# Kernel tuning notes

Measured on AMD Instinct MI355X. Metric: run time of the kernel, lower is better.

Reference implementation:

```python
import jax, jax.numpy as jnp
import numpy as np

B, NUM_ANCHORS, NUM_CLASSES = 32, 15130, 81
SCALE_XY, SCALE_WH = 0.1, 0.2
CRITERIA, MAX_OUT, SCORE_THRESH = 0.5, 200, 0.05


def setup_inputs() -> dict:
    key = jax.random.key(0)
    k1, k2, k3, k4 = jax.random.split(key, 4)
    ploc = jax.random.normal(k1, (B, 4, NUM_ANCHORS), dtype=jnp.float32)
    plabel = jax.random.normal(k2, (B, NUM_CLASSES, NUM_ANCHORS), dtype=jnp.float32)
    # default boxes in (cx, cy, w, h) form, all in [0, 1]
    xy = jax.random.uniform(k3, (NUM_ANCHORS, 2), dtype=jnp.float32, minval=0.05, maxval=0.95)
    wh = jax.random.uniform(k4, (NUM_ANCHORS, 2), dtype=jnp.float32, minval=0.02, maxval=0.3)
    dboxes_xywh = jnp.concatenate([xy, wh], axis=-1)
    return {"ploc": ploc, "plabel": plabel, "dboxes_xywh": dboxes_xywh}


def _iou(a, b):
    # a: [M,4] ltrb, b: [K,4] ltrb -> [M,K]
    lt = jnp.maximum(a[:, None, :2], b[None, :, :2])
    rb = jnp.minimum(a[:, None, 2:], b[None, :, 2:])
    wh = jnp.clip(rb - lt, 0.0)
    inter = wh[..., 0] * wh[..., 1]
    area_a = (a[:, 2] - a[:, 0]) * (a[:, 3] - a[:, 1])
    area_b = (b[:, 2] - b[:, 0]) * (b[:, 3] - b[:, 1])
    return inter / (area_a[:, None] + area_b[None, :] - inter + 1e-12)


def _decode(ploc, plabel, dboxes_xywh):
    # scale_back_batch: ploc [B,4,N] -> ltrb boxes [B,N,4]
    b = jnp.transpose(ploc, (0, 2, 1))
    xy = b[..., :2] * SCALE_XY * dboxes_xywh[:, 2:] + dboxes_xywh[:, :2]
    wh = jnp.exp(b[..., 2:] * SCALE_WH) * dboxes_xywh[:, 2:]
    ltrb = jnp.concatenate([xy - 0.5 * wh, xy + 0.5 * wh], axis=-1)  # [B,N,4]
    probs = jnp.transpose(jax.nn.softmax(plabel, axis=1), (0, 2, 1))  # [B,N,C]
    return ltrb, probs


def _nms_per_class(scores_c, boxes):
    # scores_c: [N], boxes: [N,4]
    s = jnp.where(scores_c > SCORE_THRESH, scores_c, 0.0)
    vals, idx = jax.lax.top_k(s, MAX_OUT)  # descending, matches score-sorted greedy order
    bx = boxes[idx]  # [MAX_OUT,4]
    iou = _iou(bx, bx)  # [MAX_OUT,MAX_OUT]
    later = jnp.arange(MAX_OUT)

    def body(i, keep):
        active = keep[i] & (vals[i] > 0.0)
        suppress = active & (iou[i] >= CRITERIA) & (later > i)
        return keep & ~suppress

    keep = jax.lax.fori_loop(0, MAX_OUT, body, jnp.ones((MAX_OUT,), bool))
    keep = keep & (vals > 0.0)
    return jnp.where(keep, vals, 0.0), bx


def _decode_single(probs_i, boxes_i):
    # skip background class 0
    cls_scores = probs_i[:, 1:].T  # [C-1, N]
    vals, bx = jax.vmap(_nms_per_class, in_axes=(0, None))(cls_scores, boxes_i)
    c1 = NUM_CLASSES - 1
    flat_v = vals.reshape(-1)                 # [(C-1)*MAX_OUT]
    flat_b = bx.reshape(-1, 4)
    labels = jnp.repeat(jnp.arange(1, c1 + 1, dtype=jnp.int32), MAX_OUT)
    top_v, top_i = jax.lax.top_k(flat_v, MAX_OUT)
    return flat_b[top_i], labels[top_i], top_v


def reference(ploc, plabel, dboxes_xywh):
    ltrb, probs = _decode(ploc, plabel, dboxes_xywh)
    boxes_out, labels_out, scores_out = jax.vmap(_decode_single)(probs, ltrb)
    return boxes_out, labels_out, scores_out
```

## Files before the change

### kernel.cpp

```cpp
#include <hip/hip_runtime.h>
#include <math.h>

namespace {
constexpr int BATCH = 32;
constexpr int NANCH = 15130;
constexpr int NCLS  = 81;
constexpr int C1    = 80;
constexpr int MAXO  = 200;
constexpr int APB   = 256;
constexpr int NBLKA = (NANCH + APB - 1) / APB;
constexpr int CAPK2 = 512;
constexpr int CAP   = 1024;
constexpr int CAPB  = 768;
constexpr int NBIN  = 2048;
constexpr int NBINK2 = 768;
constexpr unsigned BINBASE = 0x3D000000u;
constexpr int IMGCAP = C1 * MAXO;
}

#define SCORE_TH 0.05f
#define IOU_TH   0.5f

typedef unsigned long long u64;

__device__ __forceinline__ u64 shflx64(u64 v, int mask) {
    int lo = __shfl_xor((int)(unsigned)(v & 0xffffffffull), mask, 64);
    int hi = __shfl_xor((int)(unsigned)(v >> 32), mask, 64);
    return ((u64)(unsigned)hi << 32) | (unsigned)lo;
}

__device__ __forceinline__ void bitonic_desc(u64* keys, int P,
                                             int tid, int nthr) {
    for (int k = 2; k <= P; k <<= 1) {
        for (int j = k >> 1; j > 0; j >>= 1) {
            for (int i = tid; i < P; i += nthr) {
                int ixj = i ^ j;
                if (ixj > i) {
                    u64 a = keys[i], c = keys[ixj];
                    bool up = ((i & k) == 0);
                    if (up ? (a < c) : (a > c)) { keys[i] = c; keys[ixj] = a; }
                }
            }
            __syncthreads();
        }
    }
}

__device__ __forceinline__ u64 regsort256(u64 key, u64* lds, int tid) {
    for (int k = 2; k <= 256; k <<= 1) {
        for (int j = k >> 1; j > 0; j >>= 1) {
            u64 pv;
            if (j < 64) {
                pv = shflx64(key, j);
            } else {
                lds[tid] = key;
                __syncthreads();
                pv = lds[tid ^ j];
            }
            bool up = ((tid & k) == 0);
            bool lt = ((tid & j) == 0);
            u64 mx = (key > pv) ? key : pv;
            u64 mn = (key > pv) ? pv : key;
            key = (up == lt) ? mx : mn;
            if (j >= 64) __syncthreads();
        }
    }
    return key;
}

__device__ __forceinline__ void iou_parts(const float4 bb, const float aa,
                                          const float4 bi, const float ai,
                                          float& in_, float& dn) {
#pragma clang fp contract(off)
    float l = fmaxf(bi.x, bb.x);
    float t = fmaxf(bi.y, bb.y);
    float r = fminf(bi.z, bb.z);
    float d = fminf(bi.w, bb.w);
    in_ = fmaxf(r - l, 0.f) * fmaxf(d - t, 0.f);
    dn  = ai + aa - in_ + 1e-12f;
}

__global__ __launch_bounds__(256, 3) void ssd_decode_stats(
    const float* __restrict__ ploc, const float* __restrict__ plabel,
    const float* __restrict__ dboxes,
    float* __restrict__ ltrb, float* __restrict__ rowmax,
    float* __restrict__ rowsum,
    int* __restrict__ cntg, u64* __restrict__ bucket) {
#pragma clang fp contract(off)
    __shared__ int lcnt[C1], lbase[C1], lrank[C1];

    const int tid = threadIdx.x;
    const int b   = blockIdx.x / NBLKA;
    const int n0  = (blockIdx.x % NBLKA) * APB;
    const int n   = n0 + tid;
    const bool act = (n < NANCH);

    if (tid < C1) lcnt[tid] = 0;

    float x[NCLS];
    float s = 1.f;
    u64 w0 = 0, w1 = 0;
    if (act) {
        const float* pl = ploc + (size_t)b * 4 * NANCH + n;
        float px = pl[0], py = pl[NANCH], pw = pl[2 * NANCH],
              ph = pl[3 * NANCH];
        float4 db = reinterpret_cast<const float4*>(dboxes)[n];
        float cx = px * 0.1f * db.z + db.x;
        float cy = py * 0.1f * db.w + db.y;
        float w  = expf(pw * 0.2f) * db.z;
        float h  = expf(ph * 0.2f) * db.w;
        float4 o;
        o.x = cx - 0.5f * w; o.y = cy - 0.5f * h;
        o.z = cx + 0.5f * w; o.w = cy + 0.5f * h;
        reinterpret_cast<float4*>(ltrb)[(size_t)b * NANCH + n] = o;

        const float* pb = plabel + (size_t)b * NCLS * NANCH + n;
#pragma unroll
        for (int c = 0; c < NCLS; ++c) x[c] = pb[(size_t)c * NANCH];

        float m = -INFINITY;
#pragma unroll
        for (int c = 0; c < NCLS; ++c) m = fmaxf(m, x[c]);
#pragma unroll
        for (int c = 0; c < NCLS; ++c) x[c] = expf(x[c] - m);
        s = 0.f;
#pragma unroll
        for (int c = 0; c < NCLS; ++c) s += x[c];
        rowmax[(size_t)b * NANCH + n] = m;
        rowsum[(size_t)b * NANCH + n] = s;

        const float sc = s * SCORE_TH;
        const float lo = sc * 0.99999952f;
        const float hi = sc * 1.00000048f;
#pragma unroll
        for (int c = 1; c < NCLS; ++c) {
            float e = x[c];
            bool band = (e >= lo) && (e <= hi);
            bool pass = (e > hi);
            if (__any(band)) pass = band ? ((e / s) > SCORE_TH) : pass;
            if (pass) {
                atomicAdd(&lcnt[c - 1], 1);
                if (c <= 64) w0 |= 1ull << (c - 1);
                else         w1 |= 1ull << (c - 65);
            }
        }
    }
    __syncthreads();

    if (tid < C1) {
        int cn = lcnt[tid];
        lbase[tid] = (cn > 0) ? atomicAdd(&cntg[b * C1 + tid], cn) : 0;
        lrank[tid] = 0;
    }
    __syncthreads();

    if (act) {
#pragma unroll
        for (int c = 1; c < NCLS; ++c) {
            bool pass = (c <= 64) ? ((w0 >> (c - 1)) & 1ull)
                                  : ((w1 >> (c - 65)) & 1ull);
            if (pass) {
                int r = atomicAdd(&lrank[c - 1], 1);
                int pos = lbase[c - 1] + r;
                if (pos < CAPB) {
                    float p = x[c] / s;
                    bucket[(size_t)(b * C1 + (c - 1)) * CAPB + pos] =
                        ((u64)__float_as_uint(p) << 32)
                        | (u64)(0xFFFFFFFFu - (unsigned)n);
                }
            }
        }
    }
}

__global__ __launch_bounds__(64) void ssd_class_nms(
    const float* __restrict__ plabel, const float* __restrict__ rowmax,
    const float* __restrict__ rowsum, const float* __restrict__ ltrb,
    const int* __restrict__ cntg, const u64* __restrict__ bucket,
    float* __restrict__ pcVals, float* __restrict__ pcBoxes,
    int* __restrict__ imgcnt, u64* __restrict__ imglist) {
    __shared__ u64 pool[MAXO * 4];
    __shared__ __align__(16) u64 candbox[CAPK2];
    __shared__ int cnt, cutbin;

    unsigned* hist = (unsigned*)pool;
    u64* cand = candbox;
    float4* box4 = reinterpret_cast<float4*>(candbox);
    float* areas = reinterpret_cast<float*>(candbox) + 800;

    const int lane = threadIdx.x;
    const int b    = blockIdx.x / C1;
    const int cls  = blockIdx.x % C1 + 1;
    const int bc   = b * C1 + (cls - 1);

    for (int i = lane; i < NBINK2; i += 64) hist[i] = 0u;
    if (lane == 0) { cnt = 0; cutbin = 1; }
    __syncthreads();

    const float* pl = plabel + ((size_t)b * NCLS + cls) * NANCH;
    const float* rm = rowmax + (size_t)b * NANCH;
    const float* rs = rowsum + (size_t)b * NANCH;
    const u64* bkt = bucket + (size_t)bc * CAPB;

    const int gcount = cntg[bc];
    const bool ovf = (gcount > CAPB);
    int gathered;

    if (!ovf) {
        for (int i = lane; i < gcount; i += 64) {
            unsigned bits = (unsigned)(bkt[i] >> 32);
            unsigned bin = ((bits - BINBASE) >> 16) + 1u;
            if (bin > NBINK2 - 1) bin = NBINK2 - 1;
            atomicAdd(&hist[bin], 1u);
        }
        __syncthreads();

        const int base = lane * 12;
        int loc = 0;
#pragma unroll
        for (int k = 0; k < 12; ++k) loc += (int)hist[base + k];
        int sfx = loc;
        for (int off = 1; off < 64; off <<= 1) {
            int t = __shfl_down(sfx, off, 64);
            if (lane + off < 64) sfx += t;
        }
        const int nztot = __shfl(sfx, 0);
        {
            int S = sfx - loc;
            for (int k = 11; k >= 0; --k) {
                int binv = (int)hist[base + k];
                int Sk = S + binv;
                int bin = base + k;
                if (bin >= 1 && Sk >= MAXO && S < MAXO) cutbin = bin;
                S = Sk;
            }
        }
        __syncthreads();
        const int B = (nztot >= MAXO) ? cutbin : 1;

        for (int i = lane; i < gcount; i += 64) {
            u64 k = bkt[i];
            unsigned bits = (unsigned)(k >> 32);
            unsigned bin = ((bits - BINBASE) >> 16) + 1u;
            if (bin > NBINK2 - 1) bin = NBINK2 - 1;
            if ((int)bin >= B) {
                int pos = atomicAdd(&cnt, 1);
                if (pos < CAPK2) cand[pos] = k;
            }
        }
        __syncthreads();
        gathered = min(cnt, CAPK2);
    } else {
        for (int n = lane; n < NANCH; n += 64) {
            float p = expf(pl[n] - rm[n]) / rs[n];
            if (p > SCORE_TH) {
                int pos = atomicAdd(&cnt, 1);
                if (pos < CAPK2)
                    cand[pos] = ((u64)__float_as_uint(p) << 32)
                              | (u64)(0xFFFFFFFFu - (unsigned)n);
            }
        }
        __syncthreads();
        gathered = min(cnt, CAPK2);
    }

    u64 r0, r1, r2, r3;
    if (gathered <= 256) {
        r0 = (lane < gathered) ? cand[lane] : 0ull;
        r1 = (64 + lane < gathered) ? cand[64 + lane] : 0ull;
        r2 = (128 + lane < gathered) ? cand[128 + lane] : 0ull;
        r3 = (192 + lane < gathered) ? cand[192 + lane] : 0ull;

        auto SH = [&](u64& rr, int j, bool up) {
            u64 pv = shflx64(rr, j);
            bool lt = ((lane & j) == 0);
            u64 mx = (rr > pv) ? rr : pv;
            u64 mn = (rr > pv) ? pv : rr;
            rr = (up == lt) ? mx : mn;
        };
        auto CE = [](u64& a, u64& c, bool up) {
            u64 mx = (a > c) ? a : c;
            u64 mn = (a > c) ? c : a;
            a = up ? mx : mn;
            c = up ? mn : mx;
        };
        for (int k = 2; k <= 32; k <<= 1) {
            for (int j = k >> 1; j > 0; j >>= 1) {
                bool up = ((lane & k) == 0);
                SH(r0, j, up); SH(r1, j, up); SH(r2, j, up); SH(r3, j, up);
            }
        }
        for (int j = 32; j > 0; j >>= 1) {
            SH(r0, j, true); SH(r1, j, false); SH(r2, j, true); SH(r3, j, false);
        }
        CE(r0, r1, true); CE(r2, r3, false);
        for (int j = 32; j > 0; j >>= 1) {
            SH(r0, j, true); SH(r1, j, true); SH(r2, j, false); SH(r3, j, false);
        }
        CE(r0, r2, true); CE(r1, r3, true);
        CE(r0, r1, true); CE(r2, r3, true);
        for (int j = 32; j > 0; j >>= 1) {
            SH(r0, j, true); SH(r1, j, true); SH(r2, j, true); SH(r3, j, true);
        }
    } else {
        for (int i = gathered + lane; i < CAPK2; i += 64) cand[i] = 0ull;
        __syncthreads();
        bitonic_desc(cand, CAPK2, lane, 64);
        r0 = cand[lane]; r1 = cand[64 + lane];
        r2 = cand[128 + lane]; r3 = cand[192 + lane];
    }

    if (gathered < MAXO) {
        cand[lane] = r0; cand[64 + lane] = r1;
        cand[128 + lane] = r2; cand[192 + lane] = r3;
        __syncthreads();
        const int need = MAXO - gathered;
        int fillcnt = 0;
        for (int base2 = 0; base2 < NANCH && fillcnt < need; base2 += 64) {
            int n = base2 + lane;
            bool flag = false;
            if (n < NANCH) {
                float p = expf(pl[n] - rm[n]) / rs[n];
                flag = (p <= SCORE_TH);
            }
            u64 bal = __ballot(flag);
            u64 below = (lane == 0) ? 0ull : (~0ull >> (64 - lane));
            int excl = (int)__popcll(bal & below);
            if (flag && (fillcnt + excl) < need)
                cand[gathered + fillcnt + excl] =
                    (u64)(0xFFFFFFFFu - (unsigned)n);
            fillcnt += (int)__popcll(bal);
        }
        __syncthreads();
        r0 = cand[lane]; r1 = cand[64 + lane];
        r2 = cand[128 + lane]; r3 = cand[192 + lane];
    }

    float4 b0, b1, b2, b3;
    float a0, a1, a2, a3, v0f, v1f, v2f, v3f;
    {
#pragma clang fp contract(off)
        const float4* lt4 = reinterpret_cast<const float4*>(ltrb)
                            + (size_t)b * NANCH;
        unsigned n0_ = 0xFFFFFFFFu - (unsigned)(r0 & 0xFFFFFFFFull);
        unsigned n1_ = 0xFFFFFFFFu - (unsigned)(r1 & 0xFFFFFFFFull);
        unsigned n2_ = 0xFFFFFFFFu - (unsigned)(r2 & 0xFFFFFFFFull);
        v0f = __uint_as_float((unsigned)(r0 >> 32));
        v1f = __uint_as_float((unsigned)(r1 >> 32));
        v2f = __uint_as_float((unsigned)(r2 >> 32));
        b0 = lt4[n0_]; b1 = lt4[n1_]; b2 = lt4[n2_];
        a0 = (b0.z - b0.x) * (b0.w - b0.y);
        a1 = (b1.z - b1.x) * (b1.w - b1.y);
        a2 = (b2.z - b2.x) * (b2.w - b2.y);
        if (lane < MAXO - 192) {
            unsigned n3_ = 0xFFFFFFFFu - (unsigned)(r3 & 0xFFFFFFFFull);
            v3f = __uint_as_float((unsigned)(r3 >> 32));
            b3 = lt4[n3_];
            a3 = (b3.z - b3.x) * (b3.w - b3.y);
        } else {
            v3f = 0.f; b3 = make_float4(0.f, 0.f, 0.f, 0.f); a3 = 0.f;
        }
        __syncthreads();
        box4[lane] = b0;        areas[lane] = a0;
        box4[64 + lane] = b1;   areas[64 + lane] = a1;
        box4[128 + lane] = b2;  areas[128 + lane] = a2;
        if (lane < MAXO - 192) {
            box4[192 + lane] = b3;  areas[192 + lane] = a3;
        }
    }
    const bool j3v = (lane < MAXO - 192);
    const u64 vm0 = __ballot(v0f > 0.f);
    const u64 vm1 = __ballot(v1f > 0.f);
    const u64 vm2 = __ballot(v2f > 0.f);
    const u64 vm3 = __ballot(j3v && (v3f > 0.f));
    __syncthreads();

    u64* supflat = pool;

    u64 nz0 = 0, nz1 = 0, nz2 = 0, nz3 = 0;
    for (int i = 0; i < 64; ++i) {
#pragma clang fp contract(off)
        float4 bi = box4[i]; float ai = areas[i];
        float i0, d0_, i1, d1_, i2, d2_, i3, d3_;
        iou_parts(b0, a0, bi, ai, i0, d0_);
        iou_parts(b1, a1, bi, ai, i1, d1_);
        iou_parts(b2, a2, bi, ai, i2, d2_);
        iou_parts(b3, a3, bi, ai, i3, d3_);
        float t0 = i0 + i0, t1 = i1 + i1, t2 = i2 + i2, t3 = i3 + i3;
        bool su0 = t0 >= d0_, su1 = t1 >= d1_, su2 = t2 >= d2_, su3 = t3 >= d3_;
        bool bd0 = !su0 && (t0 > d0_ * 0.99999952f);
        bool bd1 = !su1 && (t1 > d1_ * 0.99999952f);
        bool bd2 = !su2 && (t2 > d2_ * 0.99999952f);
        bool bd3 = !su3 && (t3 > d3_ * 0.99999952f);
        if (__any(bd0 | bd1 | bd2 | bd3)) {
            su0 = bd0 ? (i0 / d0_ >= IOU_TH) : su0;
            su1 = bd1 ? (i1 / d1_ >= IOU_TH) : su1;
            su2 = bd2 ? (i2 / d2_ >= IOU_TH) : su2;
            su3 = bd3 ? (i3 / d3_ >= IOU_TH) : su3;
        }
        u64 s0 = __ballot(su0 && (lane > i));
        u64 s1 = __ballot(su1);
        u64 s2 = __ballot(su2);
        u64 s3 = __ballot(su3 && j3v);
        if ((s0 | s1 | s2 | s3) != 0ull) {
            nz0 |= 1ull << i;
            if (lane == 0) {
                supflat[i * 4 + 0] = s0; supflat[i * 4 + 1] = s1;
                supflat[i * 4 + 2] = s2; supflat[i * 4 + 3] = s3;
            }
        }
    }
    for (int i = 64; i < 128; ++i) {
#pragma clang fp contract(off)
        float4 bi = box4[i]; float ai = areas[i];
        float i1, d1_, i2, d2_, i3, d3_;
        iou_parts(b1, a1, bi, ai, i1, d1_);
        iou_parts(b2, a2, bi, ai, i2, d2_);
        iou_parts(b3, a3, bi, ai, i3, d3_);
        float t1 = i1 + i1, t2 = i2 + i2, t3 = i3 + i3;
        bool su1 = t1 >= d1_, su2 = t2 >= d2_, su3 = t3 >= d3_;
        bool bd1 = !su1 && (t1 > d1_ * 0.99999952f);
        bool bd2 = !su2 && (t2 > d2_ * 0.99999952f);
        bool bd3 = !su3 && (t3 > d3_ * 0.99999952f);
        if (__any(bd1 | bd2 | bd3)) {
            su1 = bd1 ? (i1 / d1_ >= IOU_TH) : su1;
            su2 = bd2 ? (i2 / d2_ >= IOU_TH) : su2;
            su3 = bd3 ? (i3 / d3_ >= IOU_TH) : su3;
        }
        u64 s1 = __ballot(su1 && (64 + lane > i));
        u64 s2 = __ballot(su2);
        u64 s3 = __ballot(su3 && j3v);
        if ((s1 | s2 | s3) != 0ull) {
            nz1 |= 1ull << (i - 64);
            if (lane == 0) {
                supflat[i * 4 + 1] = s1;
                supflat[i * 4 + 2] = s2; supflat[i * 4 + 3] = s3;
            }
        }
    }
    for (int i = 128; i < 192; ++i) {
#pragma clang fp contract(off)
        float4 bi = box4[i]; float ai = areas[i];
        float i2, d2_, i3, d3_;
        iou_parts(b2, a2, bi, ai, i2, d2_);
        iou_parts(b3, a3, bi, ai, i3, d3_);
        float t2 = i2 + i2, t3 = i3 + i3;
        bool su2 = t2 >= d2_, su3 = t3 >= d3_;
        bool bd2 = !su2 && (t2 > d2_ * 0.99999952f);
        bool bd3 = !su3 && (t3 > d3_ * 0.99999952f);
        if (__any(bd2 | bd3)) {
            su2 = bd2 ? (i2 / d2_ >= IOU_TH) : su2;
            su3 = bd3 ? (i3 / d3_ >= IOU_TH) : su3;
        }
        u64 s2 = __ballot(su2 && (128 + lane > i));
        u64 s3 = __ballot(su3 && j3v);
        if ((s2 | s3) != 0ull) {
            nz2 |= 1ull << (i - 128);
            if (lane == 0) {
                supflat[i * 4 + 2] = s2; supflat[i * 4 + 3] = s3;
            }
        }
    }
    for (int i = 192; i < MAXO; ++i) {
#pragma clang fp contract(off)
        float4 bi = box4[i]; float ai = areas[i];
        float i3, d3_;
        iou_parts(b3, a3, bi, ai, i3, d3_);
        float t3 = i3 + i3;
        bool su3 = t3 >= d3_;
        bool bd3 = !su3 && (t3 > d3_ * 0.99999952f);
        if (__any(bd3)) su3 = bd3 ? (i3 / d3_ >= IOU_TH) : su3;
        u64 s3 = __ballot(su3 && j3v && (192 + lane > i));
        if (s3 != 0ull) {
            nz3 |= 1ull << (i - 192);
            if (lane == 0) supflat[i * 4 + 3] = s3;
        }
    }
    __syncthreads();

    u64 k0 = ~0ull, k1 = ~0ull, k2 = ~0ull, k3 = ~0ull;
    {
        int i = -1;
        u64 c;
        if ((c = k0 & vm0 & nz0))      i = __builtin_ctzll(c);
        else if ((c = k1 & vm1 & nz1)) i = 64 + __builtin_ctzll(c);
        else if ((c = k2 & vm2 & nz2)) i = 128 + __builtin_ctzll(c);
        else if ((c = k3 & vm3 & nz3)) i = 192 + __builtin_ctzll(c);
        while (i >= 0) {
            int wr = i >> 6, bit = i & 63;
            if (wr == 0) {
                k0 &= ~supflat[i * 4 + 0]; k1 &= ~supflat[i * 4 + 1];
                k2 &= ~supflat[i * 4 + 2]; k3 &= ~supflat[i * 4 + 3];
            } else if (wr == 1) {
                k1 &= ~supflat[i * 4 + 1];
                k2 &= ~supflat[i * 4 + 2]; k3 &= ~supflat[i * 4 + 3];
            } else if (wr == 2) {
                k2 &= ~supflat[i * 4 + 2]; k3 &= ~supflat[i * 4 + 3];
            } else {
                k3 &= ~supflat[i * 4 + 3];
            }
            u64 above = (bit == 63) ? 0ull : (~0ull << (bit + 1));
            u64 cur = ((wr == 0) ? (k0 & vm0 & nz0)
                     : (wr == 1) ? (k1 & vm1 & nz1)
                     : (wr == 2) ? (k2 & vm2 & nz2)
                                 : (k3 & vm3 & nz3)) & above;
            i = -1;
            while (true) {
                if (cur) { i = wr * 64 + __builtin_ctzll(cur); break; }
                if (++wr >= 4) break;
                cur = (wr == 1) ? (k1 & vm1 & nz1)
                    : (wr == 2) ? (k2 & vm2 & nz2) : (k3 & vm3 & nz3);
            }
        }
    }

    {
        float* pv  = pcVals + (size_t)bc * MAXO;
        float4* pb4 = reinterpret_cast<float4*>(pcBoxes + (size_t)bc * MAXO * 4);
        bool kp0 = (k0 >> lane) & 1ull, kp1 = (k1 >> lane) & 1ull;
        bool kp2 = (k2 >> lane) & 1ull, kp3 = (k3 >> lane) & 1ull;
        pv[lane]        = (kp0 && v0f > 0.f) ? v0f : 0.f;
        pv[64 + lane]   = (kp1 && v1f > 0.f) ? v1f : 0.f;
        pv[128 + lane]  = (kp2 && v2f > 0.f) ? v2f : 0.f;
        pb4[lane] = b0; pb4[64 + lane] = b1; pb4[128 + lane] = b2;
        if (j3v) {
            pv[192 + lane] = (kp3 && v3f > 0.f) ? v3f : 0.f;
            pb4[192 + lane] = b3;
        }
    }

    {
        u64 km0 = k0 & vm0, km1 = k1 & vm1, km2 = k2 & vm2, km3 = k3 & vm3;
        int c0 = (int)__popcll(km0), c1 = (int)__popcll(km1);
        int c2 = (int)__popcll(km2), c3 = (int)__popcll(km3);
        int tot = c0 + c1 + c2 + c3;
        int kb = 0;
        if (lane == 0 && tot > 0) kb = atomicAdd(&imgcnt[b], tot);
        kb = __shfl(kb, 0);
        u64 below = (lane == 0) ? 0ull : (~0ull >> (64 - lane));
        u64* dst = imglist + (size_t)b * IMGCAP + kb;
        const u64 himask = 0xFFFFFFFF00000000ull;
        if ((km0 >> lane) & 1ull) {
            unsigned g = (unsigned)((cls - 1) * MAXO + lane);
            dst[__popcll(km0 & below)] =
                (r0 & himask) | (u64)(0xFFFFFFFFu - g);
        }
        if ((km1 >> lane) & 1ull) {
            unsigned g = (unsigned)((cls - 1) * MAXO + 64 + lane);
            dst[c0 + __popcll(km1 & below)] =
                (r1 & himask) | (u64)(0xFFFFFFFFu - g);
        }
        if ((km2 >> lane) & 1ull) {
            unsigned g = (unsigned)((cls - 1) * MAXO + 128 + lane);
            dst[c0 + c1 + __popcll(km2 & below)] =
                (r2 & himask) | (u64)(0xFFFFFFFFu - g);
        }
        if ((km3 >> lane) & 1ull) {
            unsigned g = (unsigned)((cls - 1) * MAXO + 192 + lane);
            dst[c0 + c1 + c2 + __popcll(km3 & below)] =
                (r3 & himask) | (u64)(0xFFFFFFFFu - g);
        }
    }
}

__global__ __launch_bounds__(256) void ssd_final_topk(
    const float* __restrict__ pcVals, const float* __restrict__ pcBoxes,
    const int* __restrict__ imgcnt, const u64* __restrict__ imglist,
    float* __restrict__ out) {
    __shared__ unsigned int hist[NBIN];
    __shared__ u64 cand[CAP];
    __shared__ int wtot[4];
    __shared__ int cnt, cutbin, nztot;

    const int tid  = threadIdx.x;
    const int lane = tid & 63;
    const int wv   = tid >> 6;
    const int b    = blockIdx.x;
    const int TOT  = C1 * MAXO;
    const float* pv = pcVals + (size_t)b * TOT;
    const int NZ   = imgcnt[b];

    for (int i = tid; i < NBIN; i += 256) hist[i] = 0u;
    if (tid == 0) { cnt = 0; cutbin = 1; }
    __syncthreads();

    int count;
    if (NZ >= MAXO) {
        const u64* lst = imglist + (size_t)b * IMGCAP;
        for (int i = tid; i < NZ; i += 256) {
            unsigned bits = (unsigned)(lst[i] >> 32);
            unsigned bin = ((bits - BINBASE) >> 15) + 1u;
            if (bin > NBIN - 1) bin = NBIN - 1;
            atomicAdd(&hist[bin], 1u);
        }
        __syncthreads();

        const int base = tid * 8;
        int loc = 0;
        for (int k = 0; k < 8; ++k) loc += (int)hist[base + k];
        int sfx = loc;
        for (int off = 1; off < 64; off <<= 1) {
            int t = __shfl_down(sfx, off, 64);
            if (lane + off < 64) sfx += t;
        }
        if (lane == 0) wtot[wv] = sfx;
        __syncthreads();
        int crossSuf = 0;
        for (int w2 = wv + 1; w2 < 4; ++w2) crossSuf += wtot[w2];
        {
            int S = (sfx - loc) + crossSuf;
            for (int k = 7; k >= 0; --k) {
                int binv = (int)hist[base + k];
                int Sk = S + binv;
                int bin = base + k;
                if (bin >= 1 && Sk >= MAXO && S < MAXO) cutbin = bin;
                S = Sk;
            }
        }
        __syncthreads();
        const int B = cutbin;

        for (int i = tid; i < NZ; i += 256) {
            u64 k = lst[i];
            unsigned bits = (unsigned)(k >> 32);
            unsigned bin = ((bits - BINBASE) >> 15) + 1u;
            if (bin > NBIN - 1) bin = NBIN - 1;
            if ((int)bin >= B) {
                int pos = atomicAdd(&cnt, 1);
                if (pos < CAP) cand[pos] = k;
            }
        }
        __syncthreads();
        count = min(cnt, CAP);
    } else {
        for (int g = tid; g < TOT; g += 256) {
            float v = pv[g];
            if (v > 0.f) {
                unsigned bits = __float_as_uint(v);
                unsigned bin = ((bits - BINBASE) >> 15) + 1u;
                if (bin > NBIN - 1) bin = NBIN - 1;
                atomicAdd(&hist[bin], 1u);
            }
        }
        __syncthreads();
        const int base = tid * 8;
        int loc = 0;
        for (int k = 0; k < 8; ++k) loc += (int)hist[base + k];
        int sfx = loc;
        for (int off = 1; off < 64; off <<= 1) {
            int t = __shfl_down(sfx, off, 64);
            if (lane + off < 64) sfx += t;
        }
        if (lane == 0) wtot[wv] = sfx;
        __syncthreads();
        int crossSuf = 0;
        for (int w2 = wv + 1; w2 < 4; ++w2) crossSuf += wtot[w2];
        if (tid == 0) nztot = wtot[0] + wtot[1] + wtot[2] + wtot[3];
        {
            int S = (sfx - loc) + crossSuf;
            for (int k = 7; k >= 0; --k) {
                int binv = (int)hist[base + k];
                int Sk = S + binv;
                int bin = base + k;
                if (bin >= 1 && Sk >= MAXO && S < MAXO) cutbin = bin;
                S = Sk;
            }
        }
        __syncthreads();
        int B = (nztot >= MAXO) ? cutbin : 1;

        for (int g = tid; g < TOT; g += 256) {
            float v = pv[g];
            if (v > 0.f) {
                unsigned bits = __float_as_uint(v);
                unsigned bin = ((bits - BINBASE) >> 15) + 1u;
                if (bin > NBIN - 1) bin = NBIN - 1;
                if ((int)bin >= B) {
                    int pos = atomicAdd(&cnt, 1);
                    if (pos < CAP)
                        cand[pos] = ((u64)bits << 32)
                                  | (u64)(0xFFFFFFFFu - (unsigned)g);
                }
            }
        }
        __syncthreads();
        count = min(cnt, CAP);

        if (count < MAXO) {
            if (tid == 0) {
                int c = count;
                for (int g = 0; g < TOT && c < MAXO; ++g) {
                    if (!(pv[g] > 0.f)) {
                        cand[c++] = (u64)(0xFFFFFFFFu - (unsigned)g);
                    }
                }
                cnt = c;
            }
            __syncthreads();
            count = min(cnt, CAP);
        }
    }

    u64 key;
    if (count <= 256) {
        key = (tid < count) ? cand[tid] : 0ull;
        key = regsort256(key, cand, tid);
    } else {
        int P = 256; while (P < count) P <<= 1;
        for (int i = count + tid; i < P; i += 256) cand[i] = 0ull;
        __syncthreads();
        bitonic_desc(cand, P, tid, 256);
        key = cand[tid];
    }

    if (tid < MAXO) {
        float sc      = __uint_as_float((unsigned)(key >> 32));
        unsigned flat = 0xFFFFFFFFu - (unsigned)(key & 0xFFFFFFFFull);
        int cls = (int)(flat / MAXO) + 1;
        const float4 bb =
            reinterpret_cast<const float4*>(pcBoxes)[(size_t)b * TOT + flat];
        reinterpret_cast<float4*>(out)[(size_t)b * MAXO + tid] = bb;
        out[(size_t)BATCH * MAXO * 4 + (size_t)b * MAXO + tid] = (float)cls;
        out[(size_t)BATCH * MAXO * 5 + (size_t)b * MAXO + tid] = sc;
    }
}

extern "C" void kernel_launch(void* const* d_in, const int* in_sizes, int n_in,
                              void* d_out, int out_size, void* d_ws,
                              size_t ws_size, hipStream_t stream) {
    const float* ploc   = (const float*)d_in[0];
    const float* plabel = (const float*)d_in[1];
    const float* dboxes = (const float*)d_in[2];
    float* out = (float*)d_out;

    float* ws      = (float*)d_ws;
    float* ltrb    = ws;
    float* rowmax  = ltrb   + (size_t)BATCH * NANCH * 4;
    float* rowsum  = rowmax + (size_t)BATCH * NANCH;
    float* pcVals  = rowsum + (size_t)BATCH * NANCH;
    float* pcBoxes = pcVals + (size_t)BATCH * C1 * MAXO;
    int*   cntg    = (int*)(pcBoxes + (size_t)BATCH * C1 * MAXO * 4);
    int*   imgcnt  = cntg + BATCH * C1;
    char*  after   = (char*)(imgcnt + BATCH);
    u64* bucket = (u64*)(after + ((16 - (((size_t)after) & 15)) & 15));
    u64* imglist = bucket + (size_t)BATCH * C1 * CAPB;

    hipMemsetAsync(cntg, 0, (size_t)(BATCH * C1 + BATCH) * sizeof(int), stream);
    ssd_decode_stats<<<BATCH * NBLKA, APB, 0, stream>>>(
        ploc, plabel, dboxes, ltrb, rowmax, rowsum, cntg, bucket);
    ssd_class_nms<<<BATCH * C1, 64, 0, stream>>>(
        plabel, rowmax, rowsum, ltrb, cntg, bucket, pcVals, pcBoxes,
        imgcnt, imglist);
    ssd_final_topk<<<BATCH, 256, 0, stream>>>(
        pcVals, pcBoxes, imgcnt, imglist, out);
}
```

Baseline: 219.2 us.

## Widen per-class NMS blocks to four wavefronts and split IoU rows across waves

The per-class NMS kernel now launches 256 threads per block instead of one 64-lane wavefront. The histogram, candidate gather, overflow scan and fill loops stride over four waves. The register bitonic sort is replaced by a 256-wide regsort helper, and the IoU suppression-mask rows are interleaved across waves with non-zero masks merged through shared atomics. The greedy bitmask walk stays on wave 0. This aims to cut per-block latency by using more lanes, but adds block-wide barriers, a barrier-heavy scan in the fill path, and three idle waves during the serial phase.

```diff
diff --git a/kernel.cpp b/kernel.cpp
--- a/kernel.cpp
+++ b/kernel.cpp
@@ -173,7 +173,7 @@
     }
 }
 
-__global__ __launch_bounds__(64) void ssd_class_nms(
+__global__ __launch_bounds__(256, 6) void ssd_class_nms(
     const float* __restrict__ plabel, const float* __restrict__ rowmax,
     const float* __restrict__ rowsum, const float* __restrict__ ltrb,
     const int* __restrict__ cntg, const u64* __restrict__ bucket,
@@ -181,20 +181,25 @@
     int* __restrict__ imgcnt, u64* __restrict__ imglist) {
     __shared__ u64 pool[MAXO * 4];
     __shared__ __align__(16) u64 candbox[CAPK2];
-    __shared__ int cnt, cutbin;
+    __shared__ u64 nzsh[4];
+    __shared__ int wtot[4];
+    __shared__ int cnt, cutbin, fillcnt;
 
     unsigned* hist = (unsigned*)pool;
     u64* cand = candbox;
     float4* box4 = reinterpret_cast<float4*>(candbox);
     float* areas = reinterpret_cast<float*>(candbox) + 800;
 
-    const int lane = threadIdx.x;
+    const int tid  = threadIdx.x;
+    const int lane = tid & 63;
+    const int wv   = tid >> 6;
     const int b    = blockIdx.x / C1;
     const int cls  = blockIdx.x % C1 + 1;
     const int bc   = b * C1 + (cls - 1);
 
-    for (int i = lane; i < NBINK2; i += 64) hist[i] = 0u;
-    if (lane == 0) { cnt = 0; cutbin = 1; }
+    for (int i = tid; i < NBINK2; i += 256) hist[i] = 0u;
+    if (tid == 0) { cnt = 0; cutbin = 1; fillcnt = 0; }
+    if (tid < 4) nzsh[tid] = 0ull;
     __syncthreads();
 
     const float* pl = plabel + ((size_t)b * NCLS + cls) * NANCH;
@@ -207,7 +212,7 @@
     int gathered;
 
     if (!ovf) {
-        for (int i = lane; i < gcount; i += 64) {
+        for (int i = tid; i < gcount; i += 256) {
             unsigned bits = (unsigned)(bkt[i] >> 32);
             unsigned bin = ((bits - BINBASE) >> 16) + 1u;
             if (bin > NBINK2 - 1) bin = NBINK2 - 1;
@@ -215,19 +220,21 @@
         }
         __syncthreads();
 
-        const int base = lane * 12;
-        int loc = 0;
-#pragma unroll
-        for (int k = 0; k < 12; ++k) loc += (int)hist[base + k];
+        const int base = tid * 3;
+        int loc = (int)hist[base] + (int)hist[base + 1] + (int)hist[base + 2];
         int sfx = loc;
         for (int off = 1; off < 64; off <<= 1) {
             int t = __shfl_down(sfx, off, 64);
             if (lane + off < 64) sfx += t;
         }
-        const int nztot = __shfl(sfx, 0);
+        if (lane == 0) wtot[wv] = sfx;
+        __syncthreads();
+        int crossSuf = 0;
+        for (int w2 = wv + 1; w2 < 4; ++w2) crossSuf += wtot[w2];
+        const int nztot = wtot[0] + wtot[1] + wtot[2] + wtot[3];
         {
-            int S = sfx - loc;
-            for (int k = 11; k >= 0; --k) {
+            int S = (sfx - loc) + crossSuf;
+            for (int k = 2; k >= 0; --k) {
                 int binv = (int)hist[base + k];
                 int Sk = S + binv;
                 int bin = base + k;
@@ -238,7 +245,7 @@
         __syncthreads();
         const int B = (nztot >= MAXO) ? cutbin : 1;
 
-        for (int i = lane; i < gcount; i += 64) {
+        for (int i = tid; i < gcount; i += 256) {
             u64 k = bkt[i];
             unsigned bits = (unsigned)(k >> 32);
             unsigned bin = ((bits - BINBASE) >> 16) + 1u;
@@ -251,7 +258,7 @@
         __syncthreads();
         gathered = min(cnt, CAPK2);
     } else {
-        for (int n = lane; n < NANCH; n += 64) {
+        for (int n = tid; n < NANCH; n += 256) {
             float p = expf(pl[n] - rm[n]) / rs[n];
             if (p > SCORE_TH) {
                 int pos = atomicAdd(&cnt, 1);
@@ -264,78 +271,52 @@
         gathered = min(cnt, CAPK2);
     }
 
-    u64 r0, r1, r2, r3;
     if (gathered <= 256) {
-        r0 = (lane < gathered) ? cand[lane] : 0ull;
-        r1 = (64 + lane < gathered) ? cand[64 + lane] : 0ull;
-        r2 = (128 + lane < gathered) ? cand[128 + lane] : 0ull;
-        r3 = (192 + lane < gathered) ? cand[192 + lane] : 0ull;
-
-        auto SH = [&](u64& rr, int j, bool up) {
-            u64 pv = shflx64(rr, j);
-            bool lt = ((lane & j) == 0);
-            u64 mx = (rr > pv) ? rr : pv;
-            u64 mn = (rr > pv) ? pv : rr;
-            rr = (up == lt) ? mx : mn;
-        };
-        auto CE = [](u64& a, u64& c, bool up) {
-            u64 mx = (a > c) ? a : c;
-            u64 mn = (a > c) ? c : a;
-            a = up ? mx : mn;
-            c = up ? mn : mx;
-        };
-        for (int k = 2; k <= 32; k <<= 1) {
-            for (int j = k >> 1; j > 0; j >>= 1) {
-                bool up = ((lane & k) == 0);
-                SH(r0, j, up); SH(r1, j, up); SH(r2, j, up); SH(r3, j, up);
-            }
-        }
-        for (int j = 32; j > 0; j >>= 1) {
-            SH(r0, j, true); SH(r1, j, false); SH(r2, j, true); SH(r3, j, false);
-        }
-        CE(r0, r1, true); CE(r2, r3, false);
-        for (int j = 32; j > 0; j >>= 1) {
-            SH(r0, j, true); SH(r1, j, true); SH(r2, j, false); SH(r3, j, false);
-        }
-        CE(r0, r2, true); CE(r1, r3, true);
-        CE(r0, r1, true); CE(r2, r3, true);
-        for (int j = 32; j > 0; j >>= 1) {
-            SH(r0, j, true); SH(r1, j, true); SH(r2, j, true); SH(r3, j, true);
-        }
+        u64 key = (tid < gathered) ? cand[tid] : 0ull;
+        key = regsort256(key, cand, tid);
+        __syncthreads();
+        cand[tid] = key;
+        if (tid < CAPK2 - 256) cand[256 + tid] = 0ull;
+        __syncthreads();
     } else {
-        for (int i = gathered + lane; i < CAPK2; i += 64) cand[i] = 0ull;
-        __syncthreads();
-        bitonic_desc(cand, CAPK2, lane, 64);
-        r0 = cand[lane]; r1 = cand[64 + lane];
-        r2 = cand[128 + lane]; r3 = cand[192 + lane];
+        for (int i = gathered + tid; i < CAPK2; i += 256) cand[i] = 0ull;
+        __syncthreads();
+        bitonic_desc(cand, CAPK2, tid, 256);
     }
 
     if (gathered < MAXO) {
-        cand[lane] = r0; cand[64 + lane] = r1;
-        cand[128 + lane] = r2; cand[192 + lane] = r3;
-        __syncthreads();
+        int* scanb = (int*)hist;
         const int need = MAXO - gathered;
-        int fillcnt = 0;
-        for (int base2 = 0; base2 < NANCH && fillcnt < need; base2 += 64) {
-            int n = base2 + lane;
-            bool flag = false;
+        for (int base2 = 0; base2 < NANCH; base2 += 256) {
+            if (fillcnt >= need) break;
+            int n = base2 + tid;
+            int flag = 0;
             if (n < NANCH) {
                 float p = expf(pl[n] - rm[n]) / rs[n];
-                flag = (p <= SCORE_TH);
-            }
-            u64 bal = __ballot(flag);
-            u64 below = (lane == 0) ? 0ull : (~0ull >> (64 - lane));
-            int excl = (int)__popcll(bal & below);
+                flag = (p <= SCORE_TH) ? 1 : 0;
+            }
+            scanb[tid] = flag;
+            __syncthreads();
+            for (int off = 1; off < 256; off <<= 1) {
+                int v  = scanb[tid];
+                int vp = (tid >= off) ? scanb[tid - off] : 0;
+                __syncthreads();
+                scanb[tid] = v + vp;
+                __syncthreads();
+            }
+            int excl = scanb[tid] - flag;
             if (flag && (fillcnt + excl) < need)
                 cand[gathered + fillcnt + excl] =
                     (u64)(0xFFFFFFFFu - (unsigned)n);
-            fillcnt += (int)__popcll(bal);
-        }
-        __syncthreads();
-        r0 = cand[lane]; r1 = cand[64 + lane];
-        r2 = cand[128 + lane]; r3 = cand[192 + lane];
-    }
-
+            __syncthreads();
+            if (tid == 0) fillcnt += scanb[255];
+            __syncthreads();
+        }
+        __syncthreads();
+    }
+
+    u64 r0 = cand[lane], r1 = cand[64 + lane];
+    u64 r2 = cand[128 + lane], r3 = cand[192 + lane];
     float4 b0, b1, b2, b3;
     float a0, a1, a2, a3, v0f, v1f, v2f, v3f;
     {
@@ -360,13 +341,13 @@
         } else {
             v3f = 0.f; b3 = make_float4(0.f, 0.f, 0.f, 0.f); a3 = 0.f;
         }
-        __syncthreads();
+    }
+    __syncthreads();
+    if (wv == 0) {
         box4[lane] = b0;        areas[lane] = a0;
         box4[64 + lane] = b1;   areas[64 + lane] = a1;
         box4[128 + lane] = b2;  areas[128 + lane] = a2;
-        if (lane < MAXO - 192) {
-            box4[192 + lane] = b3;  areas[192 + lane] = a3;
-        }
+        if (lane < MAXO - 192) { box4[192 + lane] = b3; areas[192 + lane] = a3; }
     }
     const bool j3v = (lane < MAXO - 192);
     const u64 vm0 = __ballot(v0f > 0.f);
@@ -378,7 +359,7 @@
     u64* supflat = pool;
 
     u64 nz0 = 0, nz1 = 0, nz2 = 0, nz3 = 0;
-    for (int i = 0; i < 64; ++i) {
+    for (int i = wv; i < 64; i += 4) {
 #pragma clang fp contract(off)
         float4 bi = box4[i]; float ai = areas[i];
         float i0, d0_, i1, d1_, i2, d2_, i3, d3_;
@@ -410,7 +391,7 @@
             }
         }
     }
-    for (int i = 64; i < 128; ++i) {
+    for (int i = 64 + wv; i < 128; i += 4) {
 #pragma clang fp contract(off)
         float4 bi = box4[i]; float ai = areas[i];
         float i1, d1_, i2, d2_, i3, d3_;
@@ -438,7 +419,7 @@
             }
         }
     }
-    for (int i = 128; i < 192; ++i) {
+    for (int i = 128 + wv; i < 192; i += 4) {
 #pragma clang fp contract(off)
         float4 bi = box4[i]; float ai = areas[i];
         float i2, d2_, i3, d3_;
@@ -461,7 +442,7 @@
             }
         }
     }
-    for (int i = 192; i < MAXO; ++i) {
+    for (int i = 192 + wv; i < MAXO; i += 4) {
 #pragma clang fp contract(off)
         float4 bi = box4[i]; float ai = areas[i];
         float i3, d3_;
@@ -476,16 +457,26 @@
             if (lane == 0) supflat[i * 4 + 3] = s3;
         }
     }
+    if (lane == 0) {
+        if (nz0) atomicOr(&nzsh[0], nz0);
+        if (nz1) atomicOr(&nzsh[1], nz1);
+        if (nz2) atomicOr(&nzsh[2], nz2);
+        if (nz3) atomicOr(&nzsh[3], nz3);
+    }
     __syncthreads();
+
+    if (wv != 0) return;
+
+    const u64 znz0 = nzsh[0], znz1 = nzsh[1], znz2 = nzsh[2], znz3 = nzsh[3];
 
     u64 k0 = ~0ull, k1 = ~0ull, k2 = ~0ull, k3 = ~0ull;
     {
         int i = -1;
         u64 c;
-        if ((c = k0 & vm0 & nz0))      i = __builtin_ctzll(c);
-        else if ((c = k1 & vm1 & nz1)) i = 64 + __builtin_ctzll(c);
-        else if ((c = k2 & vm2 & nz2)) i = 128 + __builtin_ctzll(c);
-        else if ((c = k3 & vm3 & nz3)) i = 192 + __builtin_ctzll(c);
+        if ((c = k0 & vm0 & znz0))      i = __builtin_ctzll(c);
+        else if ((c = k1 & vm1 & znz1)) i = 64 + __builtin_ctzll(c);
+        else if ((c = k2 & vm2 & znz2)) i = 128 + __builtin_ctzll(c);
+        else if ((c = k3 & vm3 & znz3)) i = 192 + __builtin_ctzll(c);
         while (i >= 0) {
             int wr = i >> 6, bit = i & 63;
             if (wr == 0) {
@@ -500,16 +491,16 @@
                 k3 &= ~supflat[i * 4 + 3];
             }
             u64 above = (bit == 63) ? 0ull : (~0ull << (bit + 1));
-            u64 cur = ((wr == 0) ? (k0 & vm0 & nz0)
-                     : (wr == 1) ? (k1 & vm1 & nz1)
-                     : (wr == 2) ? (k2 & vm2 & nz2)
-                                 : (k3 & vm3 & nz3)) & above;
+            u64 cur = ((wr == 0) ? (k0 & vm0 & znz0)
+                     : (wr == 1) ? (k1 & vm1 & znz1)
+                     : (wr == 2) ? (k2 & vm2 & znz2)
+                                 : (k3 & vm3 & znz3)) & above;
             i = -1;
             while (true) {
                 if (cur) { i = wr * 64 + __builtin_ctzll(cur); break; }
                 if (++wr >= 4) break;
-                cur = (wr == 1) ? (k1 & vm1 & nz1)
-                    : (wr == 2) ? (k2 & vm2 & nz2) : (k3 & vm3 & nz3);
+                cur = (wr == 1) ? (k1 & vm1 & znz1)
+                    : (wr == 2) ? (k2 & vm2 & znz2) : (k3 & vm3 & znz3);
             }
         }
     }
@@ -748,7 +739,7 @@
     hipMemsetAsync(cntg, 0, (size_t)(BATCH * C1 + BATCH) * sizeof(int), stream);
     ssd_decode_stats<<<BATCH * NBLKA, APB, 0, stream>>>(
         ploc, plabel, dboxes, ltrb, rowmax, rowsum, cntg, bucket);
-    ssd_class_nms<<<BATCH * C1, 64, 0, stream>>>(
+    ssd_class_nms<<<BATCH * C1, 256, 0, stream>>>(
         plabel, rowmax, rowsum, ltrb, cntg, bucket, pcVals, pcBoxes,
         imgcnt, imglist);
     ssd_final_topk<<<BATCH, 256, 0, stream>>>(
```

Result: faster. 194.1 us (median of 2 runs) (-11.5%).
